# Kernel tuning notes

Measured on AMD Instinct MI355X. Metric: run time of the kernel, lower is better.

The kernel has to match this reference:

```python
import jax, jax.numpy as jnp
import numpy as np

B, C, T, F = 64, 128, 2048, 5
ALPHA, BETA = 0.5, 0.5
N = C * F  # 640 nodes


def _spatial_adjacency():
    # |i-j| <= 3 neighbors within each frequency band block (block diagonal)
    idx = np.arange(C)
    d = np.abs(idx[:, None] - idx[None, :])
    blk = ((d <= 3) & (d > 0)).astype(np.float32)
    return jnp.asarray(np.kron(np.eye(F, dtype=np.float32), blk))


A_SPATIAL = _spatial_adjacency()  # (N, N)


def setup_inputs() -> dict:
    key = jax.random.key(0)
    ks = jax.random.split(key, 5)
    names = ['delta', 'theta', 'alpha', 'beta', 'gamma']
    return {n: jax.random.normal(k, (B, C, T), dtype=jnp.float32) for n, k in zip(names, ks)}


def _strg(delta, theta, alpha, beta, gamma):
    bands = jnp.stack([delta, theta, alpha, beta, gamma], axis=1)  # (B, F, C, T)
    Bn, Fn, Cn, Tn = bands.shape

    # bandpower = unbiased variance over time (torch.var default ddof=1)
    bp = jnp.var(bands, axis=3, ddof=1)  # (B, F, C)
    bandpowers = jnp.transpose(bp, (0, 2, 1))  # (B, C, F)
    # node ordering: node f*C + ch -> bandpowers[b, ch, f] == bp[b, f, ch]
    node_features = bp.reshape(Bn, Fn * Cn, 1)

    # Pearson-style functional connectivity per batch & band (vectorized)
    mean = jnp.mean(bands, axis=3, keepdims=True)
    std = jnp.std(bands, axis=3, ddof=1, keepdims=True)  # torch.std unbiased
    xn = (bands - mean) / (std + 1e-8)
    corr = jnp.einsum('bfct,bfdt->bfcd', xn, xn) / (Tn - 1)  # (B, F, C, C)
    corr = jnp.abs(corr)
    eye = jnp.eye(Cn, dtype=corr.dtype)
    corr = corr * (1.0 - eye) + eye  # zero diag, then set diag = 1
    corr = 0.5 * (corr + jnp.swapaxes(corr, 2, 3))

    # block-diagonal assembly into full functional adjacency
    A_func = jnp.zeros((Bn, N, N), dtype=corr.dtype)
    for f in range(Fn):
        s = f * Cn
        A_func = A_func.at[:, s:s + Cn, s:s + Cn].set(corr[:, f])

    A = ALPHA * A_SPATIAL[None] + BETA * A_func  # (B, N, N)

    # symmetric degree normalization D^-1/2 A D^-1/2
    D = jnp.sum(A, axis=2)
    d_inv_sqrt = (D + 1e-8) ** -0.5
    d_inv_sqrt = jnp.where(jnp.isinf(d_inv_sqrt), 0.0, d_inv_sqrt)
    A_norm = d_inv_sqrt[:, :, None] * A * d_inv_sqrt[:, None, :]

    return A_norm, node_features, bandpowers


def reference(delta, theta, alpha, beta, gamma):
    return _strg(delta, theta, alpha, beta, gamma)
```

## Files before the change

### kernel.cpp

```cpp
#include <hip/hip_runtime.h>
#include <hip/hip_bf16.h>

#define Bn 64
#define Cn 128
#define Tn 2048
#define Fn 5
#define Nn 640
#define TCHUNK 64
#define NCHUNK 32
#define BUFBYTES (Cn * TCHUNK * 2)

typedef __attribute__((ext_vector_type(8))) short bf16x8;
typedef __attribute__((ext_vector_type(4))) short bf16x4;
typedef __attribute__((ext_vector_type(4))) float f32x4;

__device__ __forceinline__ short f2bf(float f) {
    union { float f; unsigned u; } v; v.f = f;
    unsigned r = (v.u + 0x7fffu + ((v.u >> 16) & 1u)) >> 16;
    return (short)r;
}

__device__ __forceinline__ int swz(int row, int bytecol) {
    return (row * 128 + bytecol) ^ ((row & 7) << 4);
}

__device__ __forceinline__ const float* pick_band(const float* d0, const float* d1,
                                                  const float* d2, const float* d3,
                                                  const float* d4, int f) {
    return (f == 0) ? d0 : (f == 1) ? d1 : (f == 2) ? d2 : (f == 3) ? d3 : d4;
}

__global__ __launch_bounds__(512, 4)
void strg_mono(const float* __restrict__ d0, const float* __restrict__ d1,
               const float* __restrict__ d2, const float* __restrict__ d3,
               const float* __restrict__ d4, float* __restrict__ out)
{
    __shared__ __align__(16) char smem[Cn * Cn * 4];
    __shared__ float S_lds[Cn], diag[Cn], mrow[Cn], ivrow[Cn], Dsum[Cn], dinv_s[Cn];

    const int tid = threadIdx.x;
    const int bfid = blockIdx.x;
    const int b = bfid / Fn;
    const int f = bfid - b * Fn;
    const float* src = pick_band(d0, d1, d2, d3, d4, f) + (size_t)b * Cn * Tn;

    if (tid < Cn) { S_lds[tid] = 0.0f; Dsum[tid] = 0.0f; }

    const int srow = tid >> 4;
    const int sseg = tid & 15;
    const float* tb0 = src + (size_t)srow * Tn + sseg * 4;

    const int lane = tid & 63;
    const int w  = tid >> 6;
    const int wr = w >> 1;
    const int wc = w & 1;
    const int r0 = wr * 32;
    const int c0 = wc * 64;
    const int lg = lane >> 4;
    const int ll = lane & 15;

    f32x4 acc[2][4] = {};
    float psum[4] = {0.f, 0.f, 0.f, 0.f};
    float4 pfA[4], pfB[4];

    auto issueA = [&](int ch) {
        const float* cb = tb0 + ch * TCHUNK;
        #pragma unroll
        for (int i = 0; i < 4; ++i) pfA[i] = *(const float4*)(cb + (size_t)(i * 32) * Tn);
    };
    auto issueB = [&](int ch) {
        const float* cb = tb0 + ch * TCHUNK;
        #pragma unroll
        for (int i = 0; i < 4; ++i) pfB[i] = *(const float4*)(cb + (size_t)(i * 32) * Tn);
    };
    auto convA = [&](int buf) {
        char* base = smem + buf * BUFBYTES;
        #pragma unroll
        for (int i = 0; i < 4; ++i) {
            const int row = i * 32 + srow;
            float4 v = pfA[i];
            psum[i] += v.x + v.y + v.z + v.w;
            bf16x4 h; h[0] = f2bf(v.x); h[1] = f2bf(v.y); h[2] = f2bf(v.z); h[3] = f2bf(v.w);
            *(bf16x4*)(base + swz(row, sseg * 8)) = h;
        }
    };
    auto convB = [&](int buf) {
        char* base = smem + buf * BUFBYTES;
        #pragma unroll
        for (int i = 0; i < 4; ++i) {
            const int row = i * 32 + srow;
            float4 v = pfB[i];
            psum[i] += v.x + v.y + v.z + v.w;
            bf16x4 h; h[0] = f2bf(v.x); h[1] = f2bf(v.y); h[2] = f2bf(v.z); h[3] = f2bf(v.w);
            *(bf16x4*)(base + swz(row, sseg * 8)) = h;
        }
    };
    auto mfma_phase = [&](int buf) {
        const char* base = smem + buf * BUFBYTES;
        #pragma unroll
        for (int ks = 0; ks < 2; ++ks) {
            bf16x8 afr[2], bfr[4];
            #pragma unroll
            for (int m = 0; m < 2; ++m)
                afr[m] = *(const bf16x8*)(base + swz(r0 + m * 16 + ll, ks * 64 + lg * 16));
            #pragma unroll
            for (int n = 0; n < 4; ++n)
                bfr[n] = *(const bf16x8*)(base + swz(c0 + n * 16 + ll, ks * 64 + lg * 16));
            #pragma unroll
            for (int m = 0; m < 2; ++m)
                #pragma unroll
                for (int n = 0; n < 4; ++n)
                    acc[m][n] = __builtin_amdgcn_mfma_f32_16x16x32_bf16(afr[m], bfr[n], acc[m][n], 0, 0, 0);
        }
    };

    issueA(0);
    issueB(1);
    convA(0);
    issueA(2);
    asm volatile("s_waitcnt lgkmcnt(0)" ::: "memory");
    __builtin_amdgcn_s_barrier();
    __builtin_amdgcn_sched_barrier(0);

    for (int k = 0; k < NCHUNK; k += 2) {
        convB(1);
        if (k + 3 < NCHUNK) issueB(k + 3);
        mfma_phase(0);
        asm volatile("s_waitcnt lgkmcnt(0)" ::: "memory");
        __builtin_amdgcn_s_barrier();
        __builtin_amdgcn_sched_barrier(0);

        if (k + 2 < NCHUNK) {
            convA(0);
            if (k + 4 < NCHUNK) issueA(k + 4);
        }
        mfma_phase(1);
        asm volatile("s_waitcnt lgkmcnt(0)" ::: "memory");
        __builtin_amdgcn_s_barrier();
        __builtin_amdgcn_sched_barrier(0);
    }

    #pragma unroll
    for (int i = 0; i < 4; ++i)
        atomicAdd(&S_lds[i * 32 + srow], psum[i]);

    #pragma unroll
    for (int m = 0; m < 2; ++m)
      #pragma unroll
      for (int n = 0; n < 4; ++n)
        #pragma unroll
        for (int e = 0; e < 4; ++e) {
            const int row = r0 + m * 16 + lg * 4 + e;
            const int col = c0 + n * 16 + ll;
            if (row == col) diag[row] = acc[m][n][e];
        }
    __syncthreads();

    if (tid < Cn) {
        const float S  = S_lds[tid];
        const float mu = S * (1.0f / Tn);
        float var = (diag[tid] - (float)Tn * mu * mu) * (1.0f / (Tn - 1));
        var = var < 0.f ? 0.f : var;
        const float sd = sqrtf(var);
        mrow[tid]  = mu;
        ivrow[tid] = 1.0f / (sd + 1e-8f);
        const size_t ofs = (size_t)Bn * Nn * Nn;
        out[ofs + (size_t)b * Nn + f * Cn + tid] = var;
        out[ofs + (size_t)Bn * Nn + ((size_t)b * Cn + tid) * Fn + f] = var;
    }
    __syncthreads();

    float* At = (float*)smem;
    {
        float mi[2][4], ii[2][4], mj[4], ij[4];
        #pragma unroll
        for (int m = 0; m < 2; ++m)
          #pragma unroll
          for (int e = 0; e < 4; ++e) {
              const int row = r0 + m * 16 + lg * 4 + e;
              mi[m][e] = mrow[row];
              ii[m][e] = ivrow[row];
          }
        #pragma unroll
        for (int n = 0; n < 4; ++n) {
            const int col = c0 + n * 16 + ll;
            mj[n] = mrow[col];
            ij[n] = ivrow[col];
        }
        const float inv = 1.0f / (Tn - 1);
        #pragma unroll
        for (int m = 0; m < 2; ++m)
          #pragma unroll
          for (int e = 0; e < 4; ++e) {
              const int row = r0 + m * 16 + lg * 4 + e;
              float s = 0.f;
              #pragma unroll
              for (int n = 0; n < 4; ++n) {
                  const int col = c0 + n * 16 + ll;
                  float c = fabsf((acc[m][n][e] - (float)Tn * mi[m][e] * mj[n])
                                  * ii[m][e] * ij[n] * inv);
                  c = (row == col) ? 1.0f : c;
                  const int d = row > col ? row - col : col - row;
                  const float spa = (d >= 1 && d <= 3) ? 1.0f : 0.0f;
                  const float a = 0.5f * (spa + c);
                  At[row * Cn + col] = a;
                  s += a;
              }
              s += __shfl_xor(s, 1);
              s += __shfl_xor(s, 2);
              s += __shfl_xor(s, 4);
              s += __shfl_xor(s, 8);
              if (ll == 0) atomicAdd(&Dsum[row], s);
          }
    }
    __syncthreads();

    if (tid < Cn) dinv_s[tid] = rsqrtf(Dsum[tid] + 1e-8f);
    __syncthreads();

    float* Ob = out + (size_t)b * Nn * Nn;
    const int fc = f * Cn;
    for (int e = 0; e < 40; ++e) {
        const int idx4 = e * 2048 + tid * 4;
        const int row = idx4 / Nn;
        const int col = idx4 - row * Nn;
        const int cl = col - fc;
        float4 v = {0.f, 0.f, 0.f, 0.f};
        if (cl >= 0 && cl < Cn) {
            const float dr = dinv_s[row];
            v.x = dr * At[row * Cn + cl]     * dinv_s[cl];
            v.y = dr * At[row * Cn + cl + 1] * dinv_s[cl + 1];
            v.z = dr * At[row * Cn + cl + 2] * dinv_s[cl + 2];
            v.w = dr * At[row * Cn + cl + 3] * dinv_s[cl + 3];
        }
        *(float4*)(Ob + (size_t)(fc + row) * Nn + col) = v;
    }
}

extern "C" void kernel_launch(void* const* d_in, const int* in_sizes, int n_in,
                              void* d_out, int out_size, void* d_ws, size_t ws_size,
                              hipStream_t stream) {
    const float* d0 = (const float*)d_in[0];
    const float* d1 = (const float*)d_in[1];
    const float* d2 = (const float*)d_in[2];
    const float* d3 = (const float*)d_in[3];
    const float* d4 = (const float*)d_in[4];
    float* out = (float*)d_out;

    strg_mono<<<dim3(Bn * Fn), dim3(512), 0, stream>>>(d0, d1, d2, d3, d4, out);
}
```

Before: 108.6 us.

## Double time-chunk width and remap loads so each half-wave reads one row

Raises the time chunk from 64 to 128 samples, halving the number of pipeline stages and barriers, and doubles the per-thread prefetch registers. The global-load mapping is changed so each half-wave reads 512 contiguous bytes of one channel row instead of 16 threads per row. The per-row sums are now reduced with wave shuffles before a single LDS atomic per row. In exchange it uses more registers for prefetch (8 float4 per buffer), which may lower occupancy, and it doubles the LDS tile per buffer.

```diff
diff --git a/kernel.cpp b/kernel.cpp
--- a/kernel.cpp
+++ b/kernel.cpp
@@ -6,9 +6,9 @@
 #define Tn 2048
 #define Fn 5
 #define Nn 640
-#define TCHUNK 64
-#define NCHUNK 32
-#define BUFBYTES (Cn * TCHUNK * 2)
+#define TCHUNK 128
+#define NCHUNK 16
+#define BUFB (Cn * TCHUNK * 2)
 
 typedef __attribute__((ext_vector_type(8))) short bf16x8;
 typedef __attribute__((ext_vector_type(4))) short bf16x4;
@@ -21,7 +21,7 @@
 }
 
 __device__ __forceinline__ int swz(int row, int bytecol) {
-    return (row * 128 + bytecol) ^ ((row & 7) << 4);
+    return (row * 256 + bytecol) ^ ((row & 7) << 4);
 }
 
 __device__ __forceinline__ const float* pick_band(const float* d0, const float* d1,
@@ -46,12 +46,13 @@
 
     if (tid < Cn) { S_lds[tid] = 0.0f; Dsum[tid] = 0.0f; }
 
-    const int srow = tid >> 4;
-    const int sseg = tid & 15;
-    const float* tb0 = src + (size_t)srow * Tn + sseg * 4;
-
     const int lane = tid & 63;
     const int w  = tid >> 6;
+    const int half = lane >> 5;
+    const int h = lane & 31;
+    const int rbase = w * 16 + half;
+    const float* tb0 = src + (size_t)rbase * Tn + h * 4;
+
     const int wr = w >> 1;
     const int wc = w & 1;
     const int r0 = wr * 32;
@@ -60,45 +61,43 @@
     const int ll = lane & 15;
 
     f32x4 acc[2][4] = {};
-    float psum[4] = {0.f, 0.f, 0.f, 0.f};
-    float4 pfA[4], pfB[4];
+    float psum[8] = {};
+    float4 pfA[8], pfB[8];
 
     auto issueA = [&](int ch) {
         const float* cb = tb0 + ch * TCHUNK;
         #pragma unroll
-        for (int i = 0; i < 4; ++i) pfA[i] = *(const float4*)(cb + (size_t)(i * 32) * Tn);
+        for (int i = 0; i < 8; ++i) pfA[i] = *(const float4*)(cb + (size_t)(2 * i) * Tn);
     };
     auto issueB = [&](int ch) {
         const float* cb = tb0 + ch * TCHUNK;
         #pragma unroll
-        for (int i = 0; i < 4; ++i) pfB[i] = *(const float4*)(cb + (size_t)(i * 32) * Tn);
+        for (int i = 0; i < 8; ++i) pfB[i] = *(const float4*)(cb + (size_t)(2 * i) * Tn);
     };
     auto convA = [&](int buf) {
-        char* base = smem + buf * BUFBYTES;
-        #pragma unroll
-        for (int i = 0; i < 4; ++i) {
-            const int row = i * 32 + srow;
+        char* base = smem + buf * BUFB;
+        #pragma unroll
+        for (int i = 0; i < 8; ++i) {
             float4 v = pfA[i];
             psum[i] += v.x + v.y + v.z + v.w;
-            bf16x4 h; h[0] = f2bf(v.x); h[1] = f2bf(v.y); h[2] = f2bf(v.z); h[3] = f2bf(v.w);
-            *(bf16x4*)(base + swz(row, sseg * 8)) = h;
+            bf16x4 hh; hh[0] = f2bf(v.x); hh[1] = f2bf(v.y); hh[2] = f2bf(v.z); hh[3] = f2bf(v.w);
+            *(bf16x4*)(base + swz(rbase + 2 * i, h * 8)) = hh;
         }
     };
     auto convB = [&](int buf) {
-        char* base = smem + buf * BUFBYTES;
-        #pragma unroll
-        for (int i = 0; i < 4; ++i) {
-            const int row = i * 32 + srow;
+        char* base = smem + buf * BUFB;
+        #pragma unroll
+        for (int i = 0; i < 8; ++i) {
             float4 v = pfB[i];
             psum[i] += v.x + v.y + v.z + v.w;
-            bf16x4 h; h[0] = f2bf(v.x); h[1] = f2bf(v.y); h[2] = f2bf(v.z); h[3] = f2bf(v.w);
-            *(bf16x4*)(base + swz(row, sseg * 8)) = h;
+            bf16x4 hh; hh[0] = f2bf(v.x); hh[1] = f2bf(v.y); hh[2] = f2bf(v.z); hh[3] = f2bf(v.w);
+            *(bf16x4*)(base + swz(rbase + 2 * i, h * 8)) = hh;
         }
     };
     auto mfma_phase = [&](int buf) {
-        const char* base = smem + buf * BUFBYTES;
-        #pragma unroll
-        for (int ks = 0; ks < 2; ++ks) {
+        const char* base = smem + buf * BUFB;
+        #pragma unroll
+        for (int ks = 0; ks < 4; ++ks) {
             bf16x8 afr[2], bfr[4];
             #pragma unroll
             for (int m = 0; m < 2; ++m)
@@ -141,8 +140,15 @@
     }
 
     #pragma unroll
-    for (int i = 0; i < 4; ++i)
-        atomicAdd(&S_lds[i * 32 + srow], psum[i]);
+    for (int i = 0; i < 8; ++i) {
+        float s = psum[i];
+        s += __shfl_xor(s, 1);
+        s += __shfl_xor(s, 2);
+        s += __shfl_xor(s, 4);
+        s += __shfl_xor(s, 8);
+        s += __shfl_xor(s, 16);
+        if (h == 0) atomicAdd(&S_lds[rbase + 2 * i], s);
+    }
 
     #pragma unroll
     for (int m = 0; m < 2; ++m)
```

Measured after the change: 214.5 us. 1.98x slower.

## Split each batch-band block into two row halves with redundant correlation compute

Applied to the files above, without the earlier changes.

Launches twice as many blocks, and each pair redundantly computes the full 128x128 correlation. Each block then writes only its half (64 rows) of the normalized adjacency output and of the bandpower outputs. The shared staging buffer for the adjacency tile shrinks to half, lowering LDS use per block and improving grid balance across CUs. The cost is doubled input reads and doubled MFMA work.

```diff
diff --git a/kernel.cpp b/kernel.cpp
--- a/kernel.cpp
+++ b/kernel.cpp
@@ -35,11 +35,13 @@
                const float* __restrict__ d2, const float* __restrict__ d3,
                const float* __restrict__ d4, float* __restrict__ out)
 {
-    __shared__ __align__(16) char smem[Cn * Cn * 4];
+    __shared__ __align__(16) char smem[32768];
     __shared__ float S_lds[Cn], diag[Cn], mrow[Cn], ivrow[Cn], Dsum[Cn], dinv_s[Cn];
 
     const int tid = threadIdx.x;
-    const int bfid = blockIdx.x;
+    const int bx = blockIdx.x;
+    const int bfid = bx % (Bn * Fn);
+    const int h2 = bx / (Bn * Fn);
     const int b = bfid / Fn;
     const int f = bfid - b * Fn;
     const float* src = pick_band(d0, d1, d2, d3, d4, f) + (size_t)b * Cn * Tn;
@@ -80,8 +82,8 @@
             const int row = i * 32 + srow;
             float4 v = pfA[i];
             psum[i] += v.x + v.y + v.z + v.w;
-            bf16x4 h; h[0] = f2bf(v.x); h[1] = f2bf(v.y); h[2] = f2bf(v.z); h[3] = f2bf(v.w);
-            *(bf16x4*)(base + swz(row, sseg * 8)) = h;
+            bf16x4 hh; hh[0] = f2bf(v.x); hh[1] = f2bf(v.y); hh[2] = f2bf(v.z); hh[3] = f2bf(v.w);
+            *(bf16x4*)(base + swz(row, sseg * 8)) = hh;
         }
     };
     auto convB = [&](int buf) {
@@ -91,8 +93,8 @@
             const int row = i * 32 + srow;
             float4 v = pfB[i];
             psum[i] += v.x + v.y + v.z + v.w;
-            bf16x4 h; h[0] = f2bf(v.x); h[1] = f2bf(v.y); h[2] = f2bf(v.z); h[3] = f2bf(v.w);
-            *(bf16x4*)(base + swz(row, sseg * 8)) = h;
+            bf16x4 hh; hh[0] = f2bf(v.x); hh[1] = f2bf(v.y); hh[2] = f2bf(v.z); hh[3] = f2bf(v.w);
+            *(bf16x4*)(base + swz(row, sseg * 8)) = hh;
         }
     };
     auto mfma_phase = [&](int buf) {
@@ -164,9 +166,11 @@
         const float sd = sqrtf(var);
         mrow[tid]  = mu;
         ivrow[tid] = 1.0f / (sd + 1e-8f);
-        const size_t ofs = (size_t)Bn * Nn * Nn;
-        out[ofs + (size_t)b * Nn + f * Cn + tid] = var;
-        out[ofs + (size_t)Bn * Nn + ((size_t)b * Cn + tid) * Fn + f] = var;
+        if ((tid >> 6) == h2) {
+            const size_t ofs = (size_t)Bn * Nn * Nn;
+            out[ofs + (size_t)b * Nn + f * Cn + tid] = var;
+            out[ofs + (size_t)Bn * Nn + ((size_t)b * Cn + tid) * Fn + f] = var;
+        }
     }
     __syncthreads();
 
@@ -188,6 +192,7 @@
             ij[n] = ivrow[col];
         }
         const float inv = 1.0f / (Tn - 1);
+        const bool own = (wr >> 1) == h2;
         #pragma unroll
         for (int m = 0; m < 2; ++m)
           #pragma unroll
@@ -203,7 +208,7 @@
                   const int d = row > col ? row - col : col - row;
                   const float spa = (d >= 1 && d <= 3) ? 1.0f : 0.0f;
                   const float a = 0.5f * (spa + c);
-                  At[row * Cn + col] = a;
+                  if (own) At[(row - h2 * 64) * Cn + col] = a;
                   s += a;
               }
               s += __shfl_xor(s, 1);
@@ -220,20 +225,20 @@
 
     float* Ob = out + (size_t)b * Nn * Nn;
     const int fc = f * Cn;
-    for (int e = 0; e < 40; ++e) {
+    for (int e = 0; e < 20; ++e) {
         const int idx4 = e * 2048 + tid * 4;
-        const int row = idx4 / Nn;
-        const int col = idx4 - row * Nn;
+        const int rl = idx4 / Nn;
+        const int col = idx4 - rl * Nn;
         const int cl = col - fc;
         float4 v = {0.f, 0.f, 0.f, 0.f};
         if (cl >= 0 && cl < Cn) {
-            const float dr = dinv_s[row];
-            v.x = dr * At[row * Cn + cl]     * dinv_s[cl];
-            v.y = dr * At[row * Cn + cl + 1] * dinv_s[cl + 1];
-            v.z = dr * At[row * Cn + cl + 2] * dinv_s[cl + 2];
-            v.w = dr * At[row * Cn + cl + 3] * dinv_s[cl + 3];
-        }
-        *(float4*)(Ob + (size_t)(fc + row) * Nn + col) = v;
+            const float dr = dinv_s[h2 * 64 + rl];
+            v.x = dr * At[rl * Cn + cl]     * dinv_s[cl];
+            v.y = dr * At[rl * Cn + cl + 1] * dinv_s[cl + 1];
+            v.z = dr * At[rl * Cn + cl + 2] * dinv_s[cl + 2];
+            v.w = dr * At[rl * Cn + cl + 3] * dinv_s[cl + 3];
+        }
+        *(float4*)(Ob + (size_t)(fc + h2 * 64 + rl) * Nn + col) = v;
     }
 }
 
@@ -247,5 +252,5 @@
     const float* d4 = (const float*)d_in[4];
     float* out = (float*)d_out;
 
-    strg_mono<<<dim3(Bn * Fn), dim3(512), 0, stream>>>(d0, d1, d2, d3, d4, out);
-}
+    strg_mono<<<dim3(2 * Bn * Fn), dim3(512), 0, stream>>>(d0, d1, d2, d3, d4, out);
+}
```

Measured after the change: 141.7 us. 30.6% more time.

## Split into bf16 pre-convert pass and Gram kernel reading bf16 workspace

Applied to the files above, without the earlier changes.

Adds a grid-stride kernel that converts all five fp32 band inputs to bf16 into the workspace. The Gram kernel then reads half-width data in 128-sample chunks with a wider swizzle and computes the means from the bf16 values. The original monolithic kernel is kept as a fallback when the workspace is too small. This lets the 320-block Gram kernel stream fewer bytes and run fewer chunk iterations. In exchange it adds a full extra pass that reads the fp32 inputs and writes the bf16 copy, plus a second launch. Output stores are switched to nontemporal.

```diff
diff --git a/kernel.cpp b/kernel.cpp
--- a/kernel.cpp
+++ b/kernel.cpp
@@ -6,9 +6,6 @@
 #define Tn 2048
 #define Fn 5
 #define Nn 640
-#define TCHUNK 64
-#define NCHUNK 32
-#define BUFBYTES (Cn * TCHUNK * 2)
 
 typedef __attribute__((ext_vector_type(8))) short bf16x8;
 typedef __attribute__((ext_vector_type(4))) short bf16x4;
@@ -19,9 +16,9 @@
     unsigned r = (v.u + 0x7fffu + ((v.u >> 16) & 1u)) >> 16;
     return (short)r;
 }
-
-__device__ __forceinline__ int swz(int row, int bytecol) {
-    return (row * 128 + bytecol) ^ ((row & 7) << 4);
+__device__ __forceinline__ float bf2f(short h) {
+    union { unsigned u; float f; } v; v.u = ((unsigned)(unsigned short)h) << 16;
+    return v.f;
 }
 
 __device__ __forceinline__ const float* pick_band(const float* d0, const float* d1,
@@ -30,10 +27,36 @@
     return (f == 0) ? d0 : (f == 1) ? d1 : (f == 2) ? d2 : (f == 3) ? d3 : d4;
 }
 
+#define TOT_UNITS (5u * (1u << 21))
+__global__ __launch_bounds__(256)
+void k1_convert(const float* __restrict__ d0, const float* __restrict__ d1,
+                const float* __restrict__ d2, const float* __restrict__ d3,
+                const float* __restrict__ d4, short* __restrict__ wsb)
+{
+    const unsigned stride = gridDim.x * 256u;
+    for (unsigned u = blockIdx.x * 256u + threadIdx.x; u < TOT_UNITS; u += stride) {
+        const int band = u >> 21;
+        const size_t off = (size_t)(u & ((1u << 21) - 1)) * 8;
+        const float* sp = pick_band(d0, d1, d2, d3, d4, band) + off;
+        f32x4 v0 = __builtin_nontemporal_load((const f32x4*)sp);
+        f32x4 v1 = __builtin_nontemporal_load((const f32x4*)(sp + 4));
+        bf16x8 h;
+        h[0]=f2bf(v0[0]); h[1]=f2bf(v0[1]); h[2]=f2bf(v0[2]); h[3]=f2bf(v0[3]);
+        h[4]=f2bf(v1[0]); h[5]=f2bf(v1[1]); h[6]=f2bf(v1[2]); h[7]=f2bf(v1[3]);
+        *(bf16x8*)(wsb + (size_t)u * 8) = h;
+    }
+}
+
+#define TC2 128
+#define NC2 16
+#define BUF2 (Cn * TC2 * 2)
+
+__device__ __forceinline__ int swz2(int row, int bytecol) {
+    return (row * 256 + bytecol) ^ ((row & 7) << 4);
+}
+
 __global__ __launch_bounds__(512, 4)
-void strg_mono(const float* __restrict__ d0, const float* __restrict__ d1,
-               const float* __restrict__ d2, const float* __restrict__ d3,
-               const float* __restrict__ d4, float* __restrict__ out)
+void k2_gram(const short* __restrict__ wsb, float* __restrict__ out)
 {
     __shared__ __align__(16) char smem[Cn * Cn * 4];
     __shared__ float S_lds[Cn], diag[Cn], mrow[Cn], ivrow[Cn], Dsum[Cn], dinv_s[Cn];
@@ -42,13 +65,13 @@
     const int bfid = blockIdx.x;
     const int b = bfid / Fn;
     const int f = bfid - b * Fn;
-    const float* src = pick_band(d0, d1, d2, d3, d4, f) + (size_t)b * Cn * Tn;
+    const short* src = wsb + ((size_t)f * Bn + b) * (Cn * Tn);
 
     if (tid < Cn) { S_lds[tid] = 0.0f; Dsum[tid] = 0.0f; }
 
     const int srow = tid >> 4;
     const int sseg = tid & 15;
-    const float* tb0 = src + (size_t)srow * Tn + sseg * 4;
+    const short* tb0 = src + (size_t)srow * Tn + sseg * 8;
 
     const int lane = tid & 63;
     const int w  = tid >> 6;
@@ -61,51 +84,51 @@
 
     f32x4 acc[2][4] = {};
     float psum[4] = {0.f, 0.f, 0.f, 0.f};
-    float4 pfA[4], pfB[4];
+    bf16x8 pfA[4], pfB[4];
 
     auto issueA = [&](int ch) {
-        const float* cb = tb0 + ch * TCHUNK;
-        #pragma unroll
-        for (int i = 0; i < 4; ++i) pfA[i] = *(const float4*)(cb + (size_t)(i * 32) * Tn);
+        const short* cb = tb0 + ch * TC2;
+        #pragma unroll
+        for (int i = 0; i < 4; ++i) pfA[i] = *(const bf16x8*)(cb + (size_t)(i * 32) * Tn);
     };
     auto issueB = [&](int ch) {
-        const float* cb = tb0 + ch * TCHUNK;
-        #pragma unroll
-        for (int i = 0; i < 4; ++i) pfB[i] = *(const float4*)(cb + (size_t)(i * 32) * Tn);
+        const short* cb = tb0 + ch * TC2;
+        #pragma unroll
+        for (int i = 0; i < 4; ++i) pfB[i] = *(const bf16x8*)(cb + (size_t)(i * 32) * Tn);
     };
     auto convA = [&](int buf) {
-        char* base = smem + buf * BUFBYTES;
+        char* base = smem + buf * BUF2;
         #pragma unroll
         for (int i = 0; i < 4; ++i) {
             const int row = i * 32 + srow;
-            float4 v = pfA[i];
-            psum[i] += v.x + v.y + v.z + v.w;
-            bf16x4 h; h[0] = f2bf(v.x); h[1] = f2bf(v.y); h[2] = f2bf(v.z); h[3] = f2bf(v.w);
-            *(bf16x4*)(base + swz(row, sseg * 8)) = h;
+            bf16x8 hv = pfA[i];
+            psum[i] += bf2f(hv[0]) + bf2f(hv[1]) + bf2f(hv[2]) + bf2f(hv[3])
+                     + bf2f(hv[4]) + bf2f(hv[5]) + bf2f(hv[6]) + bf2f(hv[7]);
+            *(bf16x8*)(base + swz2(row, sseg * 16)) = hv;
         }
     };
     auto convB = [&](int buf) {
-        char* base = smem + buf * BUFBYTES;
+        char* base = smem + buf * BUF2;
         #pragma unroll
         for (int i = 0; i < 4; ++i) {
             const int row = i * 32 + srow;
-            float4 v = pfB[i];
-            psum[i] += v.x + v.y + v.z + v.w;
-            bf16x4 h; h[0] = f2bf(v.x); h[1] = f2bf(v.y); h[2] = f2bf(v.z); h[3] = f2bf(v.w);
-            *(bf16x4*)(base + swz(row, sseg * 8)) = h;
+            bf16x8 hv = pfB[i];
+            psum[i] += bf2f(hv[0]) + bf2f(hv[1]) + bf2f(hv[2]) + bf2f(hv[3])
+                     + bf2f(hv[4]) + bf2f(hv[5]) + bf2f(hv[6]) + bf2f(hv[7]);
+            *(bf16x8*)(base + swz2(row, sseg * 16)) = hv;
         }
     };
     auto mfma_phase = [&](int buf) {
-        const char* base = smem + buf * BUFBYTES;
-        #pragma unroll
-        for (int ks = 0; ks < 2; ++ks) {
+        const char* base = smem + buf * BUF2;
+        #pragma unroll
+        for (int ks = 0; ks < 4; ++ks) {
             bf16x8 afr[2], bfr[4];
             #pragma unroll
             for (int m = 0; m < 2; ++m)
-                afr[m] = *(const bf16x8*)(base + swz(r0 + m * 16 + ll, ks * 64 + lg * 16));
+                afr[m] = *(const bf16x8*)(base + swz2(r0 + m * 16 + ll, ks * 64 + lg * 16));
             #pragma unroll
             for (int n = 0; n < 4; ++n)
-                bfr[n] = *(const bf16x8*)(base + swz(c0 + n * 16 + ll, ks * 64 + lg * 16));
+                bfr[n] = *(const bf16x8*)(base + swz2(c0 + n * 16 + ll, ks * 64 + lg * 16));
             #pragma unroll
             for (int m = 0; m < 2; ++m)
                 #pragma unroll
@@ -122,17 +145,17 @@
     __builtin_amdgcn_s_barrier();
     __builtin_amdgcn_sched_barrier(0);
 
-    for (int k = 0; k < NCHUNK; k += 2) {
+    for (int k = 0; k < NC2; k += 2) {
         convB(1);
-        if (k + 3 < NCHUNK) issueB(k + 3);
+        if (k + 3 < NC2) issueB(k + 3);
         mfma_phase(0);
         asm volatile("s_waitcnt lgkmcnt(0)" ::: "memory");
         __builtin_amdgcn_s_barrier();
         __builtin_amdgcn_sched_barrier(0);
 
-        if (k + 2 < NCHUNK) {
+        if (k + 2 < NC2) {
             convA(0);
-            if (k + 4 < NCHUNK) issueA(k + 4);
+            if (k + 4 < NC2) issueA(k + 4);
         }
         mfma_phase(1);
         asm volatile("s_waitcnt lgkmcnt(0)" ::: "memory");
@@ -165,8 +188,8 @@
         mrow[tid]  = mu;
         ivrow[tid] = 1.0f / (sd + 1e-8f);
         const size_t ofs = (size_t)Bn * Nn * Nn;
-        out[ofs + (size_t)b * Nn + f * Cn + tid] = var;
-        out[ofs + (size_t)Bn * Nn + ((size_t)b * Cn + tid) * Fn + f] = var;
+        __builtin_nontemporal_store(var, &out[ofs + (size_t)b * Nn + f * Cn + tid]);
+        __builtin_nontemporal_store(var, &out[ofs + (size_t)Bn * Nn + ((size_t)b * Cn + tid) * Fn + f]);
     }
     __syncthreads();
 
@@ -225,6 +248,221 @@
         const int row = idx4 / Nn;
         const int col = idx4 - row * Nn;
         const int cl = col - fc;
+        f32x4 v = {0.f, 0.f, 0.f, 0.f};
+        if (cl >= 0 && cl < Cn) {
+            const float dr = dinv_s[row];
+            v[0] = dr * At[row * Cn + cl]     * dinv_s[cl];
+            v[1] = dr * At[row * Cn + cl + 1] * dinv_s[cl + 1];
+            v[2] = dr * At[row * Cn + cl + 2] * dinv_s[cl + 2];
+            v[3] = dr * At[row * Cn + cl + 3] * dinv_s[cl + 3];
+        }
+        __builtin_nontemporal_store(v, (f32x4*)(Ob + (size_t)(fc + row) * Nn + col));
+    }
+}
+
+#define TCHUNK 64
+#define NCHUNK 32
+#define BUFBYTES (Cn * TCHUNK * 2)
+
+__device__ __forceinline__ int swz(int row, int bytecol) {
+    return (row * 128 + bytecol) ^ ((row & 7) << 4);
+}
+
+__global__ __launch_bounds__(512, 4)
+void strg_mono(const float* __restrict__ d0, const float* __restrict__ d1,
+               const float* __restrict__ d2, const float* __restrict__ d3,
+               const float* __restrict__ d4, float* __restrict__ out)
+{
+    __shared__ __align__(16) char smem[Cn * Cn * 4];
+    __shared__ float S_lds[Cn], diag[Cn], mrow[Cn], ivrow[Cn], Dsum[Cn], dinv_s[Cn];
+
+    const int tid = threadIdx.x;
+    const int bfid = blockIdx.x;
+    const int b = bfid / Fn;
+    const int f = bfid - b * Fn;
+    const float* src = pick_band(d0, d1, d2, d3, d4, f) + (size_t)b * Cn * Tn;
+
+    if (tid < Cn) { S_lds[tid] = 0.0f; Dsum[tid] = 0.0f; }
+
+    const int srow = tid >> 4;
+    const int sseg = tid & 15;
+    const float* tb0 = src + (size_t)srow * Tn + sseg * 4;
+
+    const int lane = tid & 63;
+    const int w  = tid >> 6;
+    const int wr = w >> 1;
+    const int wc = w & 1;
+    const int r0 = wr * 32;
+    const int c0 = wc * 64;
+    const int lg = lane >> 4;
+    const int ll = lane & 15;
+
+    f32x4 acc[2][4] = {};
+    float psum[4] = {0.f, 0.f, 0.f, 0.f};
+    float4 pfA[4], pfB[4];
+
+    auto issueA = [&](int ch) {
+        const float* cb = tb0 + ch * TCHUNK;
+        #pragma unroll
+        for (int i = 0; i < 4; ++i) pfA[i] = *(const float4*)(cb + (size_t)(i * 32) * Tn);
+    };
+    auto issueB = [&](int ch) {
+        const float* cb = tb0 + ch * TCHUNK;
+        #pragma unroll
+        for (int i = 0; i < 4; ++i) pfB[i] = *(const float4*)(cb + (size_t)(i * 32) * Tn);
+    };
+    auto convA = [&](int buf) {
+        char* base = smem + buf * BUFBYTES;
+        #pragma unroll
+        for (int i = 0; i < 4; ++i) {
+            const int row = i * 32 + srow;
+            float4 v = pfA[i];
+            psum[i] += v.x + v.y + v.z + v.w;
+            bf16x4 hh; hh[0] = f2bf(v.x); hh[1] = f2bf(v.y); hh[2] = f2bf(v.z); hh[3] = f2bf(v.w);
+            *(bf16x4*)(base + swz(row, sseg * 8)) = hh;
+        }
+    };
+    auto convB = [&](int buf) {
+        char* base = smem + buf * BUFBYTES;
+        #pragma unroll
+        for (int i = 0; i < 4; ++i) {
+            const int row = i * 32 + srow;
+            float4 v = pfB[i];
+            psum[i] += v.x + v.y + v.z + v.w;
+            bf16x4 hh; hh[0] = f2bf(v.x); hh[1] = f2bf(v.y); hh[2] = f2bf(v.z); hh[3] = f2bf(v.w);
+            *(bf16x4*)(base + swz(row, sseg * 8)) = hh;
+        }
+    };
+    auto mfma_phase = [&](int buf) {
+        const char* base = smem + buf * BUFBYTES;
+        #pragma unroll
+        for (int ks = 0; ks < 2; ++ks) {
+            bf16x8 afr[2], bfr[4];
+            #pragma unroll
+            for (int m = 0; m < 2; ++m)
+                afr[m] = *(const bf16x8*)(base + swz(r0 + m * 16 + ll, ks * 64 + lg * 16));
+            #pragma unroll
+            for (int n = 0; n < 4; ++n)
+                bfr[n] = *(const bf16x8*)(base + swz(c0 + n * 16 + ll, ks * 64 + lg * 16));
+            #pragma unroll
+            for (int m = 0; m < 2; ++m)
+                #pragma unroll
+                for (int n = 0; n < 4; ++n)
+                    acc[m][n] = __builtin_amdgcn_mfma_f32_16x16x32_bf16(afr[m], bfr[n], acc[m][n], 0, 0, 0);
+        }
+    };
+
+    issueA(0);
+    issueB(1);
+    convA(0);
+    issueA(2);
+    asm volatile("s_waitcnt lgkmcnt(0)" ::: "memory");
+    __builtin_amdgcn_s_barrier();
+    __builtin_amdgcn_sched_barrier(0);
+
+    for (int k = 0; k < NCHUNK; k += 2) {
+        convB(1);
+        if (k + 3 < NCHUNK) issueB(k + 3);
+        mfma_phase(0);
+        asm volatile("s_waitcnt lgkmcnt(0)" ::: "memory");
+        __builtin_amdgcn_s_barrier();
+        __builtin_amdgcn_sched_barrier(0);
+
+        if (k + 2 < NCHUNK) {
+            convA(0);
+            if (k + 4 < NCHUNK) issueA(k + 4);
+        }
+        mfma_phase(1);
+        asm volatile("s_waitcnt lgkmcnt(0)" ::: "memory");
+        __builtin_amdgcn_s_barrier();
+        __builtin_amdgcn_sched_barrier(0);
+    }
+
+    #pragma unroll
+    for (int i = 0; i < 4; ++i)
+        atomicAdd(&S_lds[i * 32 + srow], psum[i]);
+
+    #pragma unroll
+    for (int m = 0; m < 2; ++m)
+      #pragma unroll
+      for (int n = 0; n < 4; ++n)
+        #pragma unroll
+        for (int e = 0; e < 4; ++e) {
+            const int row = r0 + m * 16 + lg * 4 + e;
+            const int col = c0 + n * 16 + ll;
+            if (row == col) diag[row] = acc[m][n][e];
+        }
+    __syncthreads();
+
+    if (tid < Cn) {
+        const float S  = S_lds[tid];
+        const float mu = S * (1.0f / Tn);
+        float var = (diag[tid] - (float)Tn * mu * mu) * (1.0f / (Tn - 1));
+        var = var < 0.f ? 0.f : var;
+        const float sd = sqrtf(var);
+        mrow[tid]  = mu;
+        ivrow[tid] = 1.0f / (sd + 1e-8f);
+        const size_t ofs = (size_t)Bn * Nn * Nn;
+        out[ofs + (size_t)b * Nn + f * Cn + tid] = var;
+        out[ofs + (size_t)Bn * Nn + ((size_t)b * Cn + tid) * Fn + f] = var;
+    }
+    __syncthreads();
+
+    float* At = (float*)smem;
+    {
+        float mi[2][4], ii[2][4], mj[4], ij[4];
+        #pragma unroll
+        for (int m = 0; m < 2; ++m)
+          #pragma unroll
+          for (int e = 0; e < 4; ++e) {
+              const int row = r0 + m * 16 + lg * 4 + e;
+              mi[m][e] = mrow[row];
+              ii[m][e] = ivrow[row];
+          }
+        #pragma unroll
+        for (int n = 0; n < 4; ++n) {
+            const int col = c0 + n * 16 + ll;
+            mj[n] = mrow[col];
+            ij[n] = ivrow[col];
+        }
+        const float inv = 1.0f / (Tn - 1);
+        #pragma unroll
+        for (int m = 0; m < 2; ++m)
+          #pragma unroll
+          for (int e = 0; e < 4; ++e) {
+              const int row = r0 + m * 16 + lg * 4 + e;
+              float s = 0.f;
+              #pragma unroll
+              for (int n = 0; n < 4; ++n) {
+                  const int col = c0 + n * 16 + ll;
+                  float c = fabsf((acc[m][n][e] - (float)Tn * mi[m][e] * mj[n])
+                                  * ii[m][e] * ij[n] * inv);
+                  c = (row == col) ? 1.0f : c;
+                  const int d = row > col ? row - col : col - row;
+                  const float spa = (d >= 1 && d <= 3) ? 1.0f : 0.0f;
+                  const float a = 0.5f * (spa + c);
+                  At[row * Cn + col] = a;
+                  s += a;
+              }
+              s += __shfl_xor(s, 1);
+              s += __shfl_xor(s, 2);
+              s += __shfl_xor(s, 4);
+              s += __shfl_xor(s, 8);
+              if (ll == 0) atomicAdd(&Dsum[row], s);
+          }
+    }
+    __syncthreads();
+
+    if (tid < Cn) dinv_s[tid] = rsqrtf(Dsum[tid] + 1e-8f);
+    __syncthreads();
+
+    float* Ob = out + (size_t)b * Nn * Nn;
+    const int fc = f * Cn;
+    for (int e = 0; e < 40; ++e) {
+        const int idx4 = e * 2048 + tid * 4;
+        const int row = idx4 / Nn;
+        const int col = idx4 - row * Nn;
+        const int cl = col - fc;
         float4 v = {0.f, 0.f, 0.f, 0.f};
         if (cl >= 0 && cl < Cn) {
             const float dr = dinv_s[row];
@@ -247,5 +485,12 @@
     const float* d4 = (const float*)d_in[4];
     float* out = (float*)d_out;
 
-    strg_mono<<<dim3(Bn * Fn), dim3(512), 0, stream>>>(d0, d1, d2, d3, d4, out);
-}
+    const size_t need = (size_t)5 * Bn * Cn * Tn * sizeof(short);
+    if (ws_size >= need) {
+        short* wsb = (short*)d_ws;
+        k1_convert<<<dim3(2560), dim3(256), 0, stream>>>(d0, d1, d2, d3, d4, wsb);
+        k2_gram<<<dim3(Bn * Fn), dim3(512), 0, stream>>>(wsb, out);
+    } else {
+        strg_mono<<<dim3(Bn * Fn), dim3(512), 0, stream>>>(d0, d1, d2, d3, d4, out);
+    }
+}
```

Result: slower. 160.2 us (+47.5%).
